# Performance work log

Measured on AMD Instinct MI355X. Metric: run time of the kernel, lower is better.

## Reference

```python
import jax, jax.numpy as jnp
import numpy as np

EPS = 1e-5
N_TOK = 65  # 64 chess squares + CLS


def _ln(x, g, b):
    mu = jnp.mean(x, axis=-1, keepdims=True)
    var = jnp.var(x, axis=-1, keepdims=True)
    return (x - mu) * jax.lax.rsqrt(var + EPS) * g + b


def setup_inputs() -> dict:
    key = jax.random.key(0)
    ks = jax.random.split(key, 8)
    B, N, C = 1024, N_TOK, 768
    H, D, L = 12, 64, 256
    std = 0.02
    return {
        "x": jax.random.normal(ks[0], (B, N, C), jnp.float32),
        "qkv_w": jax.random.normal(ks[1], (3 * C, C), jnp.float32) * std,
        "proj_w": jax.random.normal(ks[2], (C, C), jnp.float32) * std,
        "qn_g": jnp.ones((D,), jnp.float32),
        "qn_b": jnp.zeros((D,), jnp.float32),
        "kn_g": jnp.ones((D,), jnp.float32),
        "kn_b": jnp.zeros((D,), jnp.float32),
        "sg_w1": jax.random.normal(ks[3], (2 * L, C), jnp.float32) * std,
        "sg_ln1_g": jnp.ones((2 * L,), jnp.float32),
        "sg_ln1_b": jnp.zeros((2 * L,), jnp.float32),
        "sg_w2": jax.random.normal(ks[4], (L * H, 2 * L), jnp.float32) * std,
        "sg_ln2_g": jnp.ones((L * H,), jnp.float32),
        "sg_ln2_b": jnp.zeros((L * H,), jnp.float32),
        "sg_bias_w": jax.random.normal(ks[5], (N_TOK * N_TOK, L), jnp.float32) * std,
    }


def reference(x, qkv_w, proj_w, qn_g, qn_b, kn_g, kn_b,
              sg_w1, sg_ln1_g, sg_ln1_b, sg_w2, sg_ln2_g, sg_ln2_b, sg_bias_w):
    B, N, C = x.shape
    H = 12
    D = C // H
    L = sg_bias_w.shape[1]
    scale = D ** -0.5

    # qkv projection: [B,N,3C] -> q,k,v each [B,H,N,D]
    qkv = (x @ qkv_w.T).reshape(B, N, 3, H, D)
    qkv = jnp.transpose(qkv, (2, 0, 3, 1, 4))
    q, k, v = qkv[0], qkv[1], qkv[2]

    q = _ln(q, qn_g, qn_b) * scale
    k = _ln(k, kn_g, kn_b)

    attn = jnp.einsum('bhnd,bhmd->bhnm', q, k)

    # SmolGen dynamic per-head bias from CLS token
    cls = x[:, 0]                                  # [B,C]
    lat = jax.nn.silu(_ln(cls @ sg_w1.T, sg_ln1_g, sg_ln1_b))  # [B,2L]
    lat = _ln(lat @ sg_w2.T, sg_ln2_g, sg_ln2_b)   # [B,H*L]
    lat = lat.reshape(B, H, L)
    bias = (lat @ sg_bias_w.T).reshape(B, H, N_TOK, N_TOK)
    attn = attn + bias[:, :, :N, :N]

    attn = jax.nn.softmax(attn, axis=-1)
    out = jnp.einsum('bhnm,bhmd->bhnd', attn, v)
    out = jnp.transpose(out, (0, 2, 1, 3)).reshape(B, N, C)
    return out @ proj_w.T
```

## Files before the change

### kernel.cpp

```cpp
#include <hip/hip_runtime.h>
#include <math.h>

#define NT 65

typedef unsigned short u16;
typedef __attribute__((ext_vector_type(8))) short short8v;
typedef __attribute__((ext_vector_type(4))) float float4v;

__device__ __forceinline__ u16 bf16rn(float f) {
    unsigned int u = __float_as_uint(f);
    u += 0x7FFFu + ((u >> 16) & 1u);
    return (u16)(u >> 16);
}
__device__ __forceinline__ float bf16tof(u16 h) {
    return __uint_as_float(((unsigned int)h) << 16);
}

__device__ __forceinline__ void gload16(const void* g, void* l) {
    __builtin_amdgcn_global_load_lds(
        (const __attribute__((address_space(1))) unsigned int*)g,
        (__attribute__((address_space(3))) unsigned int*)l, 16, 0, 0);
}

__global__ __launch_bounds__(256) void gemm_bf16s(
    const u16* __restrict__ Ap, const u16* __restrict__ Wp,
    float* __restrict__ C, int N, int Kp)
{
    __shared__ __align__(16) u16 As[128 * 32];
    __shared__ __align__(16) u16 Bs[128 * 32];

    const int t = threadIdx.x;
    const int lane = t & 63, w = t >> 6;

    const int nbx = gridDim.x;
    const int nwg = nbx * gridDim.y;
    const int o   = blockIdx.y * nbx + blockIdx.x;
    const int q8  = nwg >> 3, r8 = nwg & 7;
    const int xcd = o & 7, sl = o >> 3;
    const int logical = (xcd < r8 ? xcd * (q8 + 1)
                                  : r8 * (q8 + 1) + (xcd - r8) * q8) + sl;
    const int bx = logical % nbx, by = logical / nbx;

    const int col0 = bx * 128;
    const long row0 = (long)by * 128;
    const int wm = w >> 1, wn = w & 1;

    float4v acc[4][4];
#pragma unroll
    for (int i = 0; i < 4; ++i)
#pragma unroll
        for (int j = 0; j < 4; ++j)
#pragma unroll
            for (int r = 0; r < 4; ++r) acc[i][j][r] = 0.f;

    const int srow = lane >> 2;
    const int skof = (lane & 3) * 8;

    const u16* aG0 = Ap + (row0 + w * 32 + srow) * (long)Kp + skof;
    const u16* aG1 = aG0 + 16 * (long)Kp;
    int bn0 = col0 + w * 32 + srow;      if (bn0 > N - 1) bn0 = N - 1;
    int bn1 = col0 + w * 32 + 16 + srow; if (bn1 > N - 1) bn1 = N - 1;
    const u16* bG0 = Wp + (long)bn0 * Kp + skof;
    const u16* bG1 = Wp + (long)bn1 * Kp + skof;

    u16* aL0 = &As[w * 1024];
    u16* aL1 = &As[w * 1024 + 512];
    u16* bL0 = &Bs[w * 1024];
    u16* bL1 = &Bs[w * 1024 + 512];

    const int foff = (lane & 15) * 32 + (lane >> 4) * 8;
    const u16* aF = &As[wm * 64 * 32 + foff];
    const u16* bF = &Bs[wn * 64 * 32 + foff];

    for (int kt = 0; kt < Kp; kt += 32) {
        gload16(aG0 + kt, aL0);
        gload16(aG1 + kt, aL1);
        gload16(bG0 + kt, bL0);
        gload16(bG1 + kt, bL1);
        __syncthreads();

        short8v a[4], b[4];
#pragma unroll
        for (int i = 0; i < 4; ++i) a[i] = *(const short8v*)(aF + i * 512);
#pragma unroll
        for (int j = 0; j < 4; ++j) b[j] = *(const short8v*)(bF + j * 512);
#pragma unroll
        for (int i = 0; i < 4; ++i)
#pragma unroll
            for (int j = 0; j < 4; ++j)
                acc[i][j] = __builtin_amdgcn_mfma_f32_16x16x32_bf16(
                    a[i], b[j], acc[i][j], 0, 0, 0);
        __syncthreads();
    }

    const int cn = lane & 15, cq = lane >> 4;
#pragma unroll
    for (int i = 0; i < 4; ++i) {
        const long r0 = row0 + wm * 64 + i * 16 + cq * 4;
#pragma unroll
        for (int j = 0; j < 4; ++j) {
            const int col = col0 + wn * 64 + j * 16 + cn;
            if (col < N) {
#pragma unroll
                for (int r = 0; r < 4; ++r)
                    C[(r0 + r) * (long)N + col] = acc[i][j][r];
            }
        }
    }
}

__global__ __launch_bounds__(256) void pack_split(
    const float* __restrict__ src, u16* __restrict__ dst,
    int M, int K, long rs, int wmode)
{
    const long idx = (long)blockIdx.x * 256 + threadIdx.x;
    const int k4cnt = K >> 2;
    if (idx >= (long)M * k4cnt) return;
    const int m = (int)(idx / k4cnt);
    const int k = (int)(idx % k4cnt) << 2;
    const float4 v = *(const float4*)(src + (long)m * rs + k);
    u16 h0 = bf16rn(v.x), h1 = bf16rn(v.y), h2 = bf16rn(v.z), h3 = bf16rn(v.w);
    u16 l0 = bf16rn(v.x - bf16tof(h0)), l1 = bf16rn(v.y - bf16tof(h1));
    u16 l2 = bf16rn(v.z - bf16tof(h2)), l3 = bf16rn(v.w - bf16tof(h3));
    ushort4 hv = make_ushort4(h0, h1, h2, h3);
    ushort4 lv = make_ushort4(l0, l1, l2, l3);
    u16* drow = dst + (long)m * (3 * K);
    *(ushort4*)(drow + k) = hv;
    *(ushort4*)(drow + K + k) = wmode ? lv : hv;
    *(ushort4*)(drow + 2 * K + k) = wmode ? hv : lv;
}

__global__ __launch_bounds__(256) void ln_rows(
    float* __restrict__ data, const float* __restrict__ g,
    const float* __restrict__ b, int ncols, int do_silu)
{
    const int row = blockIdx.x;
    const int t = threadIdx.x;
    float* drow = data + (long)row * ncols;

    float sum = 0.f, sumsq = 0.f;
    for (int c = t; c < ncols; c += 256) {
        float x = drow[c];
        sum += x; sumsq += x * x;
    }
#pragma unroll
    for (int off = 32; off; off >>= 1) {
        sum   += __shfl_xor(sum, off);
        sumsq += __shfl_xor(sumsq, off);
    }
    __shared__ float red[2][4];
    const int lane = t & 63, w = t >> 6;
    if (lane == 0) { red[0][w] = sum; red[1][w] = sumsq; }
    __syncthreads();
    sum   = red[0][0] + red[0][1] + red[0][2] + red[0][3];
    sumsq = red[1][0] + red[1][1] + red[1][2] + red[1][3];

    const float inv = 1.f / (float)ncols;
    const float mu  = sum * inv;
    const float var = sumsq * inv - mu * mu;
    const float r   = rsqrtf(var + 1e-5f);
    for (int c = t; c < ncols; c += 256) {
        float y = (drow[c] - mu) * r * g[c] + b[c];
        if (do_silu) y = y / (1.f + expf(-y));
        drow[c] = y;
    }
}

__global__ __launch_bounds__(256) __attribute__((amdgpu_waves_per_eu(3)))
void attn_fused(
    const float* __restrict__ qkv,
    const float* __restrict__ bias,
    const float* __restrict__ qn_g, const float* __restrict__ qn_b,
    const float* __restrict__ kn_g, const float* __restrict__ kn_b,
    float* __restrict__ attn_out)
{
    __shared__ __align__(16) float qs[NT][68];
    __shared__ __align__(16) float ks[NT][68];

    const int bh = blockIdx.x;
    const int b = bh / 12, h = bh % 12;
    const int t = threadIdx.x, lane = t & 63, w = t >> 6;
    const float scale = 0.125f;

    const float qg = qn_g[lane], qb = qn_b[lane];
    const float kg = kn_g[lane], kb = kn_b[lane];
    const float* base = qkv + (long)(b * NT) * 2304 + h * 64;

    for (int n = w; n < NT; n += 4) {
        const float* row = base + (long)n * 2304;
        float qv = row[lane];
        float kv = row[768 + lane];

        float s = qv;
#pragma unroll
        for (int off = 32; off; off >>= 1) s += __shfl_xor(s, off);
        float mu = s * (1.f / 64.f);
        float dq = qv - mu;
        float s2 = dq * dq;
#pragma unroll
        for (int off = 32; off; off >>= 1) s2 += __shfl_xor(s2, off);
        qs[n][lane] = (dq * rsqrtf(s2 * (1.f / 64.f) + 1e-5f) * qg + qb) * scale;

        s = kv;
#pragma unroll
        for (int off = 32; off; off >>= 1) s += __shfl_xor(s, off);
        mu = s * (1.f / 64.f);
        float dk = kv - mu;
        s2 = dk * dk;
#pragma unroll
        for (int off = 32; off; off >>= 1) s2 += __shfl_xor(s2, off);
        ks[n][lane] = dk * rsqrtf(s2 * (1.f / 64.f) + 1e-5f) * kg + kb;
    }
    __syncthreads();

    const int tx = t & 15, ty = t >> 4;
    const int n0 = ty * 4, m0 = tx * 4;
    const float* brow = bias + (long)bh * 4225;

    float acc[4][4];
#pragma unroll
    for (int i = 0; i < 4; ++i)
#pragma unroll
        for (int j = 0; j < 4; ++j) acc[i][j] = 0.f;

#pragma unroll 2
    for (int d = 0; d < 64; d += 4) {
        float qa[4][4], ka[4][4];
#pragma unroll
        for (int i = 0; i < 4; ++i) {
            float4 tmp = *(const float4*)&qs[n0 + i][d];
            qa[i][0] = tmp.x; qa[i][1] = tmp.y; qa[i][2] = tmp.z; qa[i][3] = tmp.w;
        }
#pragma unroll
        for (int j = 0; j < 4; ++j) {
            float4 tmp = *(const float4*)&ks[m0 + j][d];
            ka[j][0] = tmp.x; ka[j][1] = tmp.y; ka[j][2] = tmp.z; ka[j][3] = tmp.w;
        }
#pragma unroll
        for (int i = 0; i < 4; ++i)
#pragma unroll
            for (int j = 0; j < 4; ++j)
#pragma unroll
                for (int k = 0; k < 4; ++k)
                    acc[i][j] = fmaf(qa[i][k], ka[j][k], acc[i][j]);
    }
#pragma unroll
    for (int i = 0; i < 4; ++i)
#pragma unroll
        for (int j = 0; j < 4; ++j)
            acc[i][j] += brow[(n0 + i) * 65 + (m0 + j)];

    float eacc = 0.f;
    int en = 0, em = 0;
    if (t < 129) {
        en = (t < 65) ? 64 : (t - 65);
        em = (t < 65) ? t  : 64;
#pragma unroll 4
        for (int d = 0; d < 64; d += 4) {
            float4 qa4 = *(const float4*)&qs[en][d];
            float4 ka4 = *(const float4*)&ks[em][d];
            eacc += qa4.x * ka4.x + qa4.y * ka4.y + qa4.z * ka4.z + qa4.w * ka4.w;
        }
        eacc += brow[en * 65 + em];
    }
    __syncthreads();

    float (*ps)[68] = qs;
    float (*vsd)[68] = ks;
#pragma unroll
    for (int i = 0; i < 4; ++i)
#pragma unroll
        for (int j = 0; j < 4; ++j)
            ps[n0 + i][m0 + j] = acc[i][j];
    if (t < 129) ps[en][em] = eacc;
    __syncthreads();

    for (int n = w; n < NT; n += 4) {
        float vv = base[(long)n * 2304 + 1536 + lane];
        float v0 = ps[n][lane];
        float v1 = (lane == 0) ? ps[n][64] : -1e30f;
        float mx = fmaxf(v0, v1);
#pragma unroll
        for (int off = 32; off; off >>= 1) mx = fmaxf(mx, __shfl_xor(mx, off));
        float e0 = __expf(v0 - mx);
        float e1 = (lane == 0) ? __expf(v1 - mx) : 0.f;
        float sm = e0 + e1;
#pragma unroll
        for (int off = 32; off; off >>= 1) sm += __shfl_xor(sm, off);
        float inv = 1.f / sm;
        ps[n][lane] = e0 * inv;
        if (lane == 0) ps[n][64] = e1 * inv;
        vsd[n][lane] = vv;
    }
    __syncthreads();

    const int d0 = tx * 4;
    float o[4][4];
#pragma unroll
    for (int i = 0; i < 4; ++i)
#pragma unroll
        for (int j = 0; j < 4; ++j) o[i][j] = 0.f;

#pragma unroll 2
    for (int m = 0; m < 64; m += 4) {
        float pa[4][4], va[4][4];
#pragma unroll
        for (int i = 0; i < 4; ++i) {
            float4 tmp = *(const float4*)&ps[n0 + i][m];
            pa[i][0] = tmp.x; pa[i][1] = tmp.y; pa[i][2] = tmp.z; pa[i][3] = tmp.w;
        }
#pragma unroll
        for (int jj = 0; jj < 4; ++jj) {
            float4 tmp = *(const float4*)&vsd[m + jj][d0];
            va[jj][0] = tmp.x; va[jj][1] = tmp.y; va[jj][2] = tmp.z; va[jj][3] = tmp.w;
        }
#pragma unroll
        for (int i = 0; i < 4; ++i)
#pragma unroll
            for (int k = 0; k < 4; ++k)
#pragma unroll
                for (int j = 0; j < 4; ++j)
                    o[i][j] = fmaf(pa[i][k], va[k][j], o[i][j]);
    }
#pragma unroll
    for (int i = 0; i < 4; ++i) {
        float p64 = ps[n0 + i][64];
#pragma unroll
        for (int j = 0; j < 4; ++j)
            o[i][j] = fmaf(p64, vsd[64][d0 + j], o[i][j]);
    }

    const long outbase = (long)(b * NT) * 768 + h * 64;
#pragma unroll
    for (int i = 0; i < 4; ++i)
        *(float4*)&attn_out[outbase + (long)(n0 + i) * 768 + d0] =
            make_float4(o[i][0], o[i][1], o[i][2], o[i][3]);

    if (t < 16) {
        const int dd = t * 4;
        float oo0 = 0.f, oo1 = 0.f, oo2 = 0.f, oo3 = 0.f;
        for (int m = 0; m < NT; ++m) {
            float p = ps[64][m];
            oo0 = fmaf(p, vsd[m][dd + 0], oo0);
            oo1 = fmaf(p, vsd[m][dd + 1], oo1);
            oo2 = fmaf(p, vsd[m][dd + 2], oo2);
            oo3 = fmaf(p, vsd[m][dd + 3], oo3);
        }
        *(float4*)&attn_out[outbase + 64L * 768 + dd] = make_float4(oo0, oo1, oo2, oo3);
    }
}

extern "C" void kernel_launch(void* const* d_in, const int* in_sizes, int n_in,
                              void* d_out, int out_size, void* d_ws, size_t ws_size,
                              hipStream_t stream)
{
    const float* x         = (const float*)d_in[0];
    const float* qkv_w     = (const float*)d_in[1];
    const float* proj_w    = (const float*)d_in[2];
    const float* qn_g      = (const float*)d_in[3];
    const float* qn_b      = (const float*)d_in[4];
    const float* kn_g      = (const float*)d_in[5];
    const float* kn_b      = (const float*)d_in[6];
    const float* sg_w1     = (const float*)d_in[7];
    const float* sg_ln1_g  = (const float*)d_in[8];
    const float* sg_ln1_b  = (const float*)d_in[9];
    const float* sg_w2     = (const float*)d_in[10];
    const float* sg_ln2_g  = (const float*)d_in[11];
    const float* sg_ln2_b  = (const float*)d_in[12];
    const float* sg_bias_w = (const float*)d_in[13];
    float* out = (float*)d_out;

    const int Bc = 256, nchunk = 4;
    const long Mq = (long)Bc * NT;

    float* ws     = (float*)d_ws;
    float* qkv_c  = ws;
    float* bias_c = qkv_c  + 38338560L;
    float* aout_c = bias_c + 12979200L;
    float* lat1   = aout_c + 12779520L;
    float* lat2   = lat1   + 524288L;
    u16*   P1     = (u16*)(lat2 + 3145728L);
    u16*   clsp   = P1     + 38338560L;
    u16*   lat1p  = clsp   + 2359296L;
    u16*   lat2p  = lat1p  + 1572864L;
    u16*   qkvwp  = lat2p  + 9437184L;
    u16*   projwp = qkvwp  + 5308416L;
    u16*   sgw1p  = projwp + 1769472L;
    u16*   sgw2p  = sgw1p  + 1179648L;
    u16*   sgbwp  = sgw2p  + 4718592L;

    pack_split<<<(2304 * 192 + 255) / 256, 256, 0, stream>>>(qkv_w, qkvwp, 2304, 768, 768, 1);
    pack_split<<<( 768 * 192 + 255) / 256, 256, 0, stream>>>(proj_w, projwp, 768, 768, 768, 1);
    pack_split<<<( 512 * 192 + 255) / 256, 256, 0, stream>>>(sg_w1, sgw1p, 512, 768, 768, 1);
    pack_split<<<(3072 * 128 + 255) / 256, 256, 0, stream>>>(sg_w2, sgw2p, 3072, 512, 512, 1);
    pack_split<<<(4225 *  64 + 255) / 256, 256, 0, stream>>>(sg_bias_w, sgbwp, 4225, 256, 256, 1);

    pack_split<<<(1024 * 192 + 255) / 256, 256, 0, stream>>>(x, clsp, 1024, 768, (long)NT * 768, 0);
    gemm_bf16s<<<dim3(512 / 128, 1024 / 128), 256, 0, stream>>>(clsp, sgw1p, lat1, 512, 2304);
    ln_rows<<<1024, 256, 0, stream>>>(lat1, sg_ln1_g, sg_ln1_b, 512, 1);
    pack_split<<<(1024 * 128 + 255) / 256, 256, 0, stream>>>(lat1, lat1p, 1024, 512, 512, 0);
    gemm_bf16s<<<dim3(3072 / 128, 1024 / 128), 256, 0, stream>>>(lat1p, sgw2p, lat2, 3072, 1536);
    ln_rows<<<1024, 256, 0, stream>>>(lat2, sg_ln2_g, sg_ln2_b, 3072, 0);
    pack_split<<<(12288 * 64 + 255) / 256, 256, 0, stream>>>(lat2, lat2p, 12288, 256, 256, 0);

    for (int c = 0; c < nchunk; ++c) {
        const float* xc = x + (long)c * Mq * 768;

        pack_split<<<(int)((Mq * 192 + 255) / 256), 256, 0, stream>>>(xc, P1, (int)Mq, 768, 768, 0);
        gemm_bf16s<<<dim3(2304 / 128, (int)(Mq / 128)), 256, 0, stream>>>(P1, qkvwp, qkv_c, 2304, 2304);
        gemm_bf16s<<<dim3((4225 + 127) / 128, 3072 / 128), 256, 0, stream>>>(
            lat2p + (long)c * 3072 * 768, sgbwp, bias_c, 4225, 768);
        attn_fused<<<Bc * 12, 256, 0, stream>>>(qkv_c, bias_c, qn_g, qn_b, kn_g, kn_b, aout_c);
        pack_split<<<(int)((Mq * 192 + 255) / 256), 256, 0, stream>>>(aout_c, P1, (int)Mq, 768, 768, 0);
        gemm_bf16s<<<dim3(768 / 128, (int)(Mq / 128)), 256, 0, stream>>>(
            P1, projwp, out + (long)c * Mq * 768, 768, 2304);
    }
}
```

Baseline: 2.935 ms.

## Double-buffer GEMM LDS tiles and stride attention key columns to avoid bank conflicts

The bf16 GEMM now uses two LDS buffers per operand and issues the global-to-LDS loads for the next K tile before the MFMAs on the current one. This overlaps memory latency with compute and leaves one barrier per iteration instead of two. Separately, the attention score tile maps each thread's key columns as tx+16*j instead of four consecutive columns, so LDS reads of ks and writes of ps hit different banks. LDS usage for the GEMM doubles, which may lower occupancy.

```diff
diff --git a/kernel.cpp b/kernel.cpp
--- a/kernel.cpp
+++ b/kernel.cpp
@@ -26,8 +26,8 @@
     const u16* __restrict__ Ap, const u16* __restrict__ Wp,
     float* __restrict__ C, int N, int Kp)
 {
-    __shared__ __align__(16) u16 As[128 * 32];
-    __shared__ __align__(16) u16 Bs[128 * 32];
+    __shared__ __align__(16) u16 As[2][128 * 32];
+    __shared__ __align__(16) u16 Bs[2][128 * 32];
 
     const int t = threadIdx.x;
     const int lane = t & 63, w = t >> 6;
@@ -63,22 +63,26 @@
     const u16* bG0 = Wp + (long)bn0 * Kp + skof;
     const u16* bG1 = Wp + (long)bn1 * Kp + skof;
 
-    u16* aL0 = &As[w * 1024];
-    u16* aL1 = &As[w * 1024 + 512];
-    u16* bL0 = &Bs[w * 1024];
-    u16* bL1 = &Bs[w * 1024 + 512];
-
     const int foff = (lane & 15) * 32 + (lane >> 4) * 8;
-    const u16* aF = &As[wm * 64 * 32 + foff];
-    const u16* bF = &Bs[wn * 64 * 32 + foff];
-
+
+    gload16(aG0, &As[0][w * 1024]);
+    gload16(aG1, &As[0][w * 1024 + 512]);
+    gload16(bG0, &Bs[0][w * 1024]);
+    gload16(bG1, &Bs[0][w * 1024 + 512]);
+    __syncthreads();
+
+    int cur = 0;
     for (int kt = 0; kt < Kp; kt += 32) {
-        gload16(aG0 + kt, aL0);
-        gload16(aG1 + kt, aL1);
-        gload16(bG0 + kt, bL0);
-        gload16(bG1 + kt, bL1);
-        __syncthreads();
-
+        if (kt + 32 < Kp) {
+            const int nxt = cur ^ 1;
+            gload16(aG0 + kt + 32, &As[nxt][w * 1024]);
+            gload16(aG1 + kt + 32, &As[nxt][w * 1024 + 512]);
+            gload16(bG0 + kt + 32, &Bs[nxt][w * 1024]);
+            gload16(bG1 + kt + 32, &Bs[nxt][w * 1024 + 512]);
+        }
+
+        const u16* aF = &As[cur][wm * 64 * 32 + foff];
+        const u16* bF = &Bs[cur][wn * 64 * 32 + foff];
         short8v a[4], b[4];
 #pragma unroll
         for (int i = 0; i < 4; ++i) a[i] = *(const short8v*)(aF + i * 512);
@@ -90,7 +94,9 @@
             for (int j = 0; j < 4; ++j)
                 acc[i][j] = __builtin_amdgcn_mfma_f32_16x16x32_bf16(
                     a[i], b[j], acc[i][j], 0, 0, 0);
+
         __syncthreads();
+        cur ^= 1;
     }
 
     const int cn = lane & 15, cq = lane >> 4;
@@ -214,7 +220,7 @@
     __syncthreads();
 
     const int tx = t & 15, ty = t >> 4;
-    const int n0 = ty * 4, m0 = tx * 4;
+    const int n0 = ty * 4;
     const float* brow = bias + (long)bh * 4225;
 
     float acc[4][4];
@@ -233,7 +239,7 @@
         }
 #pragma unroll
         for (int j = 0; j < 4; ++j) {
-            float4 tmp = *(const float4*)&ks[m0 + j][d];
+            float4 tmp = *(const float4*)&ks[tx + 16 * j][d];
             ka[j][0] = tmp.x; ka[j][1] = tmp.y; ka[j][2] = tmp.z; ka[j][3] = tmp.w;
         }
 #pragma unroll
@@ -248,7 +254,7 @@
     for (int i = 0; i < 4; ++i)
 #pragma unroll
         for (int j = 0; j < 4; ++j)
-            acc[i][j] += brow[(n0 + i) * 65 + (m0 + j)];
+            acc[i][j] += brow[(n0 + i) * 65 + tx + 16 * j];
 
     float eacc = 0.f;
     int en = 0, em = 0;
@@ -271,7 +277,7 @@
     for (int i = 0; i < 4; ++i)
 #pragma unroll
         for (int j = 0; j < 4; ++j)
-            ps[n0 + i][m0 + j] = acc[i][j];
+            ps[n0 + i][tx + 16 * j] = acc[i][j];
     if (t < 129) ps[en][em] = eacc;
     __syncthreads();
 
```

After: 2.507 ms. -14.6%, faster.
